# Kernel optimization log

Measured on AMD Instinct MI355X. Metric: run time of the kernel, lower is better.

The kernel has to match this reference:

```python
import jax, jax.numpy as jnp
import numpy as np

N_NODES = 170000
N_EDGES = 1200000
IN_DIM = 64
OUT_DIM = 40


def setup_inputs() -> dict:
    key = jax.random.key(0)
    k1, k2, k3, k4 = jax.random.split(key, 4)
    feats = jax.random.normal(k1, (N_NODES, IN_DIM), dtype=jnp.float32)
    # Linear layer params (Kaiming-ish scale)
    W = jax.random.normal(k2, (OUT_DIM, IN_DIM), dtype=jnp.float32) * (1.0 / np.sqrt(IN_DIM))
    b = jnp.zeros((OUT_DIM,), dtype=jnp.float32)
    src = jax.random.randint(k3, (N_EDGES,), 0, N_NODES, dtype=jnp.int64)
    dst = jax.random.randint(k4, (N_EDGES,), 0, N_NODES, dtype=jnp.int64)
    return {"feats": feats, "W": W, "b": b, "src": src, "dst": dst}


def reference(feats, W, b, src, dst):
    # DGL SGConv, k=1: symmetric normalization by in-degree^-1/2 on both sides.
    n = feats.shape[0]
    deg = jax.ops.segment_sum(jnp.ones_like(dst, dtype=feats.dtype), dst, num_segments=n)
    norm = jax.lax.rsqrt(jnp.maximum(deg, 1.0))  # clamp(min=1)
    h = feats * norm[:, None]                    # [N, D] pre-scale
    msgs = jnp.take(h, src, axis=0)              # [E, D] gather
    agg = jax.ops.segment_sum(msgs, dst, num_segments=n)  # [N, D] scatter-sum
    h = agg * norm[:, None]                      # post-scale
    out = jnp.einsum('nd,cd->nc', h, W) + b      # Linear(IN_DIM -> OUT_DIM)
    return out
```

## Files before the change

kernel.cpp:

```cpp
#include <hip/hip_runtime.h>
#include <hip/hip_bf16.h>

#define N_NODES 170000
#define N_EDGES 1200000
#define IN_DIM 64
#define OUT_DIM 40
#define PAD 32
#define ZW 20
#define MTILES (N_NODES / 16)
#define TFB ((MTILES + 3) / 4)
#define SEGS 8
#define SEG_SZ (N_NODES / SEGS)
#define SLICES 512
#define SLICE_E ((N_EDGES + SLICES - 1) / SLICES)
#define FILLB (SLICES * SEGS)
#define FUSED_BLOCKS (FILLB + TFB)
#define GWAVES (N_NODES / 2)
#define WS_DS32_OFF 36056576ULL
#define WS_SS32_OFF (WS_DS32_OFF + (size_t)N_EDGES * 4)
#define WS_NEED     (WS_SS32_OFF + (size_t)N_EDGES * 4)

typedef __attribute__((ext_vector_type(8))) short short8;
typedef __attribute__((ext_vector_type(4))) float f32x4;

__device__ __forceinline__ float bf2f(unsigned int u) {
    union { unsigned int i; float f; } v;
    v.i = u << 16;
    return v.f;
}

__device__ __forceinline__ unsigned short f2bf_bits(float x) {
    __hip_bfloat16 h = __float2bfloat16(x);
    union { __hip_bfloat16 h; unsigned short u; } c; c.h = h;
    return c.u;
}

__device__ __forceinline__ int load_idx(const void* p, int e, int is_i32) {
    return is_i32 ? ((const int*)p)[e] : (int)((const long long*)p)[e];
}

__global__ void __launch_bounds__(256) k_init(
    const unsigned short* __restrict__ Wraw, const unsigned short* __restrict__ braw,
    const unsigned int* __restrict__ dstraw, const unsigned int* __restrict__ srcraw,
    int* __restrict__ flags, unsigned short* __restrict__ Wb, float* __restrict__ bfv,
    int* __restrict__ cnt, int* __restrict__ ds32, int* __restrict__ ss32) {
    int tid = blockIdx.x * 256 + threadIdx.x;
    int gsz = (int)gridDim.x * 256;
    int4* c4 = (int4*)cnt;
    for (int i = tid; i < 42500; i += gsz) c4[i] = make_int4(0, 0, 0, 0);

    __shared__ int s_i32l;
    if (threadIdx.x == 0) s_i32l = 0;
    __syncthreads();
    if (dstraw[2 * threadIdx.x + 1] != 0u) atomicOr(&s_i32l, 1);
    __syncthreads();
    int is_i32 = s_i32l;

    if (!is_i32 && ds32) {
        const long long* d64 = (const long long*)dstraw;
        const long long* s64 = (const long long*)srcraw;
        for (int i = tid; i < N_EDGES; i += gsz) ds32[i] = (int)d64[i];
        for (int i = tid; i < N_EDGES; i += gsz) ss32[i] = (int)s64[i];
    }
    if (blockIdx.x != 0) return;

    __shared__ int s_f32;
    if (threadIdx.x == 0) s_f32 = 0;
    __syncthreads();
    for (int i = threadIdx.x; i < OUT_DIM * IN_DIM; i += 256) {
        float v = bf2f(Wraw[i]);
        if (!(fabsf(v) <= 100.0f)) atomicOr(&s_f32, 1);
    }
    __syncthreads();
    int is_f32 = s_f32;
    if (threadIdx.x == 0) { flags[0] = s_f32; flags[1] = is_i32; }
    for (int i = threadIdx.x; i < OUT_DIM * IN_DIM; i += 256)
        Wb[i] = is_f32 ? f2bf_bits(((const float*)Wraw)[i]) : Wraw[i];
    for (int i = threadIdx.x; i < OUT_DIM; i += 256)
        bfv[i] = is_f32 ? ((const float*)braw)[i] : bf2f(braw[i]);
}

__global__ void __launch_bounds__(256) k_fused(
    const void* __restrict__ src, const void* __restrict__ dst,
    int* __restrict__ cnt, int* __restrict__ slots,
    const void* __restrict__ feats, const unsigned short* __restrict__ Wb,
    unsigned short* __restrict__ Zp16, const int* __restrict__ flags,
    const int* __restrict__ ds32, const int* __restrict__ ss32) {
    int bid = blockIdx.x;
    int do_fill, id;
    if (bid < 2 * TFB) { do_fill = bid & 1; id = bid >> 1; }
    else               { do_fill = 1;       id = bid - TFB; }

    if (do_fill) {
        int is_i32 = flags[1];
        int seg   = id & 7;
        int slice = id >> 3;
        int lo = seg * SEG_SZ, hi = lo + SEG_SZ;
        int e0 = slice * SLICE_E;
        int e1 = e0 + SLICE_E; if (e1 > N_EDGES) e1 = N_EDGES;
        const int* dp = is_i32 ? (const int*)dst : ds32;
        const int* sp = is_i32 ? (const int*)src : ss32;
        if (dp) {
            int nE = e1 - e0;
            int nV = nE >> 2;
            const int4* dv = (const int4*)(dp + e0);
            const int4* sv = (const int4*)(sp + e0);
            for (int q = (int)threadIdx.x; q < nV; q += 256) {
                int4 d4 = dv[q];
                int4 s4 = sv[q];
                if (d4.x >= lo && d4.x < hi) {
                    int pos = atomicAdd(&cnt[d4.x], 1);
                    if (pos < PAD) slots[(size_t)d4.x * PAD + pos] = s4.x;
                }
                if (d4.y >= lo && d4.y < hi) {
                    int pos = atomicAdd(&cnt[d4.y], 1);
                    if (pos < PAD) slots[(size_t)d4.y * PAD + pos] = s4.y;
                }
                if (d4.z >= lo && d4.z < hi) {
                    int pos = atomicAdd(&cnt[d4.z], 1);
                    if (pos < PAD) slots[(size_t)d4.z * PAD + pos] = s4.z;
                }
                if (d4.w >= lo && d4.w < hi) {
                    int pos = atomicAdd(&cnt[d4.w], 1);
                    if (pos < PAD) slots[(size_t)d4.w * PAD + pos] = s4.w;
                }
            }
            int rem = nE & 3;
            if ((int)threadIdx.x < rem) {
                int e = e0 + (nV << 2) + (int)threadIdx.x;
                int d = dp[e];
                if (d >= lo && d < hi) {
                    int pos = atomicAdd(&cnt[d], 1);
                    if (pos < PAD) slots[(size_t)d * PAD + pos] = sp[e];
                }
            }
        } else {
            for (int e = e0 + (int)threadIdx.x; e < e1; e += 256) {
                int d = load_idx(dst, e, 0);
                if (d >= lo && d < hi) {
                    int s = load_idx(src, e, 0);
                    int pos = atomicAdd(&cnt[d], 1);
                    if (pos < PAD) slots[(size_t)d * PAD + pos] = s;
                }
            }
        }
    } else {
        int is_f32 = flags[0];
        int wave = id * 4 + (int)(threadIdx.x >> 6);
        int lane = threadIdx.x & 63;
        if (wave >= MTILES) return;
        int m = lane & 15;
        int quad = lane >> 4;
        int node0 = wave * 16;

        short8 a0, a1;
        if (is_f32) {
            const float* frow = (const float*)feats + (size_t)(node0 + m) * IN_DIM + quad * 8;
            float4 p0 = *(const float4*)(frow + 0);
            float4 p1 = *(const float4*)(frow + 4);
            float4 p2 = *(const float4*)(frow + 32);
            float4 p3 = *(const float4*)(frow + 36);
            a0[0] = (short)f2bf_bits(p0.x); a0[1] = (short)f2bf_bits(p0.y);
            a0[2] = (short)f2bf_bits(p0.z); a0[3] = (short)f2bf_bits(p0.w);
            a0[4] = (short)f2bf_bits(p1.x); a0[5] = (short)f2bf_bits(p1.y);
            a0[6] = (short)f2bf_bits(p1.z); a0[7] = (short)f2bf_bits(p1.w);
            a1[0] = (short)f2bf_bits(p2.x); a1[1] = (short)f2bf_bits(p2.y);
            a1[2] = (short)f2bf_bits(p2.z); a1[3] = (short)f2bf_bits(p2.w);
            a1[4] = (short)f2bf_bits(p3.x); a1[5] = (short)f2bf_bits(p3.y);
            a1[6] = (short)f2bf_bits(p3.z); a1[7] = (short)f2bf_bits(p3.w);
        } else {
            const unsigned short* frow = (const unsigned short*)feats + (size_t)(node0 + m) * IN_DIM + quad * 8;
            a0 = *(const short8*)(frow);
            a1 = *(const short8*)(frow + 32);
        }

        f32x4 c0 = {0.f, 0.f, 0.f, 0.f}, c1 = c0, c2 = c0;
#pragma unroll
        for (int t = 0; t < 3; t++) {
            int n = t * 16 + m;
            bool ok = (n < OUT_DIM);
            short8 b0, b1;
#pragma unroll
            for (int j = 0; j < 8; j++) { b0[j] = 0; b1[j] = 0; }
            if (ok) {
                const unsigned short* wrow = Wb + (size_t)n * IN_DIM + quad * 8;
                b0 = *(const short8*)(wrow);
                b1 = *(const short8*)(wrow + 32);
            }
            if (t == 0) {
                c0 = __builtin_amdgcn_mfma_f32_16x16x32_bf16(a0, b0, c0, 0, 0, 0);
                c0 = __builtin_amdgcn_mfma_f32_16x16x32_bf16(a1, b1, c0, 0, 0, 0);
            } else if (t == 1) {
                c1 = __builtin_amdgcn_mfma_f32_16x16x32_bf16(a0, b0, c1, 0, 0, 0);
                c1 = __builtin_amdgcn_mfma_f32_16x16x32_bf16(a1, b1, c1, 0, 0, 0);
            } else {
                c2 = __builtin_amdgcn_mfma_f32_16x16x32_bf16(a0, b0, c2, 0, 0, 0);
                c2 = __builtin_amdgcn_mfma_f32_16x16x32_bf16(a1, b1, c2, 0, 0, 0);
            }
        }

        int r0 = quad * 4;
#pragma unroll
        for (int r = 0; r < 4; r++) {
            size_t base = (size_t)(node0 + r0 + r) * OUT_DIM;
            Zp16[base + m]      = f2bf_bits(c0[r]);
            Zp16[base + 16 + m] = f2bf_bits(c1[r]);
            if (m < 8)
                Zp16[base + 32 + m] = f2bf_bits(c2[r]);
        }
    }
}

__global__ void __launch_bounds__(256) k_gather(
    const int* __restrict__ cnt, const int* __restrict__ slots,
    const unsigned int* __restrict__ Zp, const float* __restrict__ bfv,
    float* __restrict__ out) {
    int wid = (blockIdx.x * blockDim.x + threadIdx.x) >> 6;
    int lane = threadIdx.x & 63;
    if (wid >= GWAVES) return;
    int nA = wid * 2, nB = nA + 1;

    int deg_my = cnt[nA + (lane >> 5)];
    int deg_ot = __shfl(deg_my, lane ^ 32);
    int degA = (lane < 32) ? deg_my : deg_ot;
    int degB = (lane < 32) ? deg_ot : deg_my;
    int dcA = degA > PAD ? PAD : degA;
    int dcB = degB > PAD ? PAD : degB;
    int dcm = dcA > dcB ? dcA : dcB;

    int myslot = slots[(size_t)(nA + (lane >> 5)) * PAD + (lane & 31)];

    int grp = lane / 10;
    int g3 = grp - (grp >= 3 ? 3 : 0);
    int cidx = lane - grp * 10;
    bool lact = (grp < 6);
    int side = (grp >= 3);
    int dcS = side ? dcB : dcA;
    int sbase = side * 32;

    float a0 = 0.f, a1 = 0.f, a2 = 0.f, a3 = 0.f;
    if (dcm > 0) {
        int rounds = (dcm + 2) / 3;
        int e = g3;
        bool v = lact && (e < dcS);
        int s = __shfl(myslot, sbase + (v ? e : 0));
        s = v ? s : 0;
        uint2 r = *(const uint2*)(Zp + (size_t)s * ZW + 2 * cidx);
        int cdeg = cnt[s];
        for (int rd = 1; rd < rounds; rd++) {
            int e1 = rd * 3 + g3;
            bool v1 = lact && (e1 < dcS);
            int s1 = __shfl(myslot, sbase + (v1 ? e1 : 0));
            s1 = v1 ? s1 : 0;
            uint2 rn = *(const uint2*)(Zp + (size_t)s1 * ZW + 2 * cidx);
            int cn = cnt[s1];
            if (v) {
                float nvs = rsqrtf(cdeg > 1 ? (float)cdeg : 1.0f);
                a0 = fmaf(bf2f(r.x & 0xFFFFu), nvs, a0);
                a1 = fmaf(bf2f(r.x >> 16),     nvs, a1);
                a2 = fmaf(bf2f(r.y & 0xFFFFu), nvs, a2);
                a3 = fmaf(bf2f(r.y >> 16),     nvs, a3);
            }
            v = v1; r = rn; cdeg = cn;
        }
        if (v) {
            float nvs = rsqrtf(cdeg > 1 ? (float)cdeg : 1.0f);
            a0 = fmaf(bf2f(r.x & 0xFFFFu), nvs, a0);
            a1 = fmaf(bf2f(r.x >> 16),     nvs, a1);
            a2 = fmaf(bf2f(r.y & 0xFFFFu), nvs, a2);
            a3 = fmaf(bf2f(r.y >> 16),     nvs, a3);
        }
    }
    float t0 = a0 + __shfl(a0, (lane + 10) & 63) + __shfl(a0, (lane + 20) & 63);
    float t1 = a1 + __shfl(a1, (lane + 10) & 63) + __shfl(a1, (lane + 20) & 63);
    float t2 = a2 + __shfl(a2, (lane + 10) & 63) + __shfl(a2, (lane + 20) & 63);
    float t3 = a3 + __shfl(a3, (lane + 10) & 63) + __shfl(a3, (lane + 20) & 63);

    bool wA = (lane < 10);
    bool wB = (lane >= 30 && lane < 40);
    if (wA || wB) {
        int nOut = wA ? nA : nB;
        int ci   = wA ? lane : (lane - 30);
        int dg   = wA ? degA : degB;
        float nv = rsqrtf(dg > 1 ? (float)dg : 1.0f);
        float4 o;
        o.x = fmaf(t0, nv, bfv[4 * ci + 0]);
        o.y = fmaf(t1, nv, bfv[4 * ci + 1]);
        o.z = fmaf(t2, nv, bfv[4 * ci + 2]);
        o.w = fmaf(t3, nv, bfv[4 * ci + 3]);
        *reinterpret_cast<float4*>(out + (size_t)nOut * OUT_DIM + 4 * ci) = o;
    }
}

extern "C" void kernel_launch(void* const* d_in, const int* in_sizes, int n_in,
                              void* d_out, int out_size, void* d_ws, size_t ws_size,
                              hipStream_t stream) {
    const void* feats = d_in[0];
    const void* W     = d_in[1];
    const void* b     = d_in[2];
    const void* src   = d_in[3];
    const void* dst   = d_in[4];

    char* ws = (char*)d_ws;
    int*            flags = (int*)(ws + 0);
    float*          bfv   = (float*)(ws + 256);
    unsigned short* Wb    = (unsigned short*)(ws + 1024);
    int*            cnt   = (int*)(ws + 16384);
    int*            slots = (int*)(ws + 696448);
    unsigned short* Zp16  = (unsigned short*)(ws + 22456448);
    unsigned int*   Zp    = (unsigned int*)(ws + 22456448);
    int*            ds32  = (ws_size >= WS_NEED) ? (int*)(ws + WS_DS32_OFF) : nullptr;
    int*            ss32  = (ws_size >= WS_NEED) ? (int*)(ws + WS_SS32_OFF) : nullptr;

    k_init<<<1024, 256, 0, stream>>>((const unsigned short*)W, (const unsigned short*)b,
                                     (const unsigned int*)dst, (const unsigned int*)src,
                                     flags, Wb, bfv, cnt, ds32, ss32);
    k_fused<<<FUSED_BLOCKS, 256, 0, stream>>>(src, dst, cnt, slots, feats, Wb, Zp16, flags, ds32, ss32);
    k_gather<<<(GWAVES * 64 + 255) / 256, 256, 0, stream>>>(cnt, slots, Zp, bfv, (float*)d_out);
}
```

Baseline: 196.5 us.

## Merge init, fill/transform, and gather into one cooperative persistent kernel

```diff
diff --git a/kernel.cpp b/kernel.cpp
--- a/kernel.cpp
+++ b/kernel.cpp
@@ -1,5 +1,8 @@
 #include <hip/hip_runtime.h>
 #include <hip/hip_bf16.h>
+#include <hip/hip_cooperative_groups.h>
+
+namespace cg = cooperative_groups;
 
 #define N_NODES 170000
 #define N_EDGES 1200000
@@ -14,8 +17,9 @@
 #define SLICES 512
 #define SLICE_E ((N_EDGES + SLICES - 1) / SLICES)
 #define FILLB (SLICES * SEGS)
-#define FUSED_BLOCKS (FILLB + TFB)
+#define FUSED_UNITS (FILLB + TFB)
 #define GWAVES (N_NODES / 2)
+#define GCHUNKS (GWAVES / 4)
 #define WS_DS32_OFF 36056576ULL
 #define WS_SS32_OFF (WS_DS32_OFF + (size_t)N_EDGES * 4)
 #define WS_NEED     (WS_SS32_OFF + (size_t)N_EDGES * 4)
@@ -39,185 +43,134 @@
     return is_i32 ? ((const int*)p)[e] : (int)((const long long*)p)[e];
 }
 
-__global__ void __launch_bounds__(256) k_init(
-    const unsigned short* __restrict__ Wraw, const unsigned short* __restrict__ braw,
-    const unsigned int* __restrict__ dstraw, const unsigned int* __restrict__ srcraw,
-    int* __restrict__ flags, unsigned short* __restrict__ Wb, float* __restrict__ bfv,
-    int* __restrict__ cnt, int* __restrict__ ds32, int* __restrict__ ss32) {
-    int tid = blockIdx.x * 256 + threadIdx.x;
-    int gsz = (int)gridDim.x * 256;
-    int4* c4 = (int4*)cnt;
-    for (int i = tid; i < 42500; i += gsz) c4[i] = make_int4(0, 0, 0, 0);
-
-    __shared__ int s_i32l;
-    if (threadIdx.x == 0) s_i32l = 0;
-    __syncthreads();
-    if (dstraw[2 * threadIdx.x + 1] != 0u) atomicOr(&s_i32l, 1);
-    __syncthreads();
-    int is_i32 = s_i32l;
-
-    if (!is_i32 && ds32) {
-        const long long* d64 = (const long long*)dstraw;
-        const long long* s64 = (const long long*)srcraw;
-        for (int i = tid; i < N_EDGES; i += gsz) ds32[i] = (int)d64[i];
-        for (int i = tid; i < N_EDGES; i += gsz) ss32[i] = (int)s64[i];
-    }
-    if (blockIdx.x != 0) return;
-
-    __shared__ int s_f32;
-    if (threadIdx.x == 0) s_f32 = 0;
-    __syncthreads();
-    for (int i = threadIdx.x; i < OUT_DIM * IN_DIM; i += 256) {
-        float v = bf2f(Wraw[i]);
-        if (!(fabsf(v) <= 100.0f)) atomicOr(&s_f32, 1);
-    }
-    __syncthreads();
-    int is_f32 = s_f32;
-    if (threadIdx.x == 0) { flags[0] = s_f32; flags[1] = is_i32; }
-    for (int i = threadIdx.x; i < OUT_DIM * IN_DIM; i += 256)
-        Wb[i] = is_f32 ? f2bf_bits(((const float*)Wraw)[i]) : Wraw[i];
-    for (int i = threadIdx.x; i < OUT_DIM; i += 256)
-        bfv[i] = is_f32 ? ((const float*)braw)[i] : bf2f(braw[i]);
-}
-
-__global__ void __launch_bounds__(256) k_fused(
-    const void* __restrict__ src, const void* __restrict__ dst,
-    int* __restrict__ cnt, int* __restrict__ slots,
-    const void* __restrict__ feats, const unsigned short* __restrict__ Wb,
-    unsigned short* __restrict__ Zp16, const int* __restrict__ flags,
-    const int* __restrict__ ds32, const int* __restrict__ ss32) {
-    int bid = blockIdx.x;
-    int do_fill, id;
-    if (bid < 2 * TFB) { do_fill = bid & 1; id = bid >> 1; }
-    else               { do_fill = 1;       id = bid - TFB; }
-
-    if (do_fill) {
-        int is_i32 = flags[1];
-        int seg   = id & 7;
-        int slice = id >> 3;
-        int lo = seg * SEG_SZ, hi = lo + SEG_SZ;
-        int e0 = slice * SLICE_E;
-        int e1 = e0 + SLICE_E; if (e1 > N_EDGES) e1 = N_EDGES;
-        const int* dp = is_i32 ? (const int*)dst : ds32;
-        const int* sp = is_i32 ? (const int*)src : ss32;
-        if (dp) {
-            int nE = e1 - e0;
-            int nV = nE >> 2;
-            const int4* dv = (const int4*)(dp + e0);
-            const int4* sv = (const int4*)(sp + e0);
-            for (int q = (int)threadIdx.x; q < nV; q += 256) {
-                int4 d4 = dv[q];
-                int4 s4 = sv[q];
-                if (d4.x >= lo && d4.x < hi) {
-                    int pos = atomicAdd(&cnt[d4.x], 1);
-                    if (pos < PAD) slots[(size_t)d4.x * PAD + pos] = s4.x;
-                }
-                if (d4.y >= lo && d4.y < hi) {
-                    int pos = atomicAdd(&cnt[d4.y], 1);
-                    if (pos < PAD) slots[(size_t)d4.y * PAD + pos] = s4.y;
-                }
-                if (d4.z >= lo && d4.z < hi) {
-                    int pos = atomicAdd(&cnt[d4.z], 1);
-                    if (pos < PAD) slots[(size_t)d4.z * PAD + pos] = s4.z;
-                }
-                if (d4.w >= lo && d4.w < hi) {
-                    int pos = atomicAdd(&cnt[d4.w], 1);
-                    if (pos < PAD) slots[(size_t)d4.w * PAD + pos] = s4.w;
-                }
-            }
-            int rem = nE & 3;
-            if ((int)threadIdx.x < rem) {
-                int e = e0 + (nV << 2) + (int)threadIdx.x;
-                int d = dp[e];
-                if (d >= lo && d < hi) {
-                    int pos = atomicAdd(&cnt[d], 1);
-                    if (pos < PAD) slots[(size_t)d * PAD + pos] = sp[e];
-                }
-            }
+
+__device__ __forceinline__ void fill_unit(
+    int id, int is_i32, const void* src, const void* dst,
+    const int* dp_, const int* sp_, int* cnt, int* slots) {
+    int seg   = id & 7;
+    int slice = id >> 3;
+    int lo = seg * SEG_SZ, hi = lo + SEG_SZ;
+    int e0 = slice * SLICE_E;
+    int e1 = e0 + SLICE_E; if (e1 > N_EDGES) e1 = N_EDGES;
+    const int* dp = is_i32 ? (const int*)dst : dp_;
+    const int* sp = is_i32 ? (const int*)src : sp_;
+    if (dp) {
+        int nE = e1 - e0;
+        int nV = nE >> 2;
+        const int4* dv = (const int4*)(dp + e0);
+        const int4* sv = (const int4*)(sp + e0);
+        for (int q = (int)threadIdx.x; q < nV; q += 256) {
+            int4 d4 = dv[q];
+            int4 s4 = sv[q];
+            if (d4.x >= lo && d4.x < hi) {
+                int pos = atomicAdd(&cnt[d4.x], 1);
+                if (pos < PAD) slots[(size_t)d4.x * PAD + pos] = s4.x;
+            }
+            if (d4.y >= lo && d4.y < hi) {
+                int pos = atomicAdd(&cnt[d4.y], 1);
+                if (pos < PAD) slots[(size_t)d4.y * PAD + pos] = s4.y;
+            }
+            if (d4.z >= lo && d4.z < hi) {
+                int pos = atomicAdd(&cnt[d4.z], 1);
+                if (pos < PAD) slots[(size_t)d4.z * PAD + pos] = s4.z;
+            }
+            if (d4.w >= lo && d4.w < hi) {
+                int pos = atomicAdd(&cnt[d4.w], 1);
+                if (pos < PAD) slots[(size_t)d4.w * PAD + pos] = s4.w;
+            }
+        }
+        int rem = nE & 3;
+        if ((int)threadIdx.x < rem) {
+            int e = e0 + (nV << 2) + (int)threadIdx.x;
+            int d = dp[e];
+            if (d >= lo && d < hi) {
+                int pos = atomicAdd(&cnt[d], 1);
+                if (pos < PAD) slots[(size_t)d * PAD + pos] = sp[e];
+            }
+        }
+    } else {
+        for (int e = e0 + (int)threadIdx.x; e < e1; e += 256) {
+            int d = load_idx(dst, e, 0);
+            if (d >= lo && d < hi) {
+                int s = load_idx(src, e, 0);
+                int pos = atomicAdd(&cnt[d], 1);
+                if (pos < PAD) slots[(size_t)d * PAD + pos] = s;
+            }
+        }
+    }
+}
+
+__device__ __forceinline__ void transform_unit(
+    int id, int is_f32, const void* feats, const unsigned short* Wb,
+    unsigned short* Zp16) {
+    int wave = id * 4 + (int)(threadIdx.x >> 6);
+    int lane = threadIdx.x & 63;
+    if (wave >= MTILES) return;
+    int m = lane & 15;
+    int quad = lane >> 4;
+    int node0 = wave * 16;
+
+    short8 a0, a1;
+    if (is_f32) {
+        const float* frow = (const float*)feats + (size_t)(node0 + m) * IN_DIM + quad * 8;
+        float4 p0 = *(const float4*)(frow + 0);
+        float4 p1 = *(const float4*)(frow + 4);
+        float4 p2 = *(const float4*)(frow + 32);
+        float4 p3 = *(const float4*)(frow + 36);
+        a0[0] = (short)f2bf_bits(p0.x); a0[1] = (short)f2bf_bits(p0.y);
+        a0[2] = (short)f2bf_bits(p0.z); a0[3] = (short)f2bf_bits(p0.w);
+        a0[4] = (short)f2bf_bits(p1.x); a0[5] = (short)f2bf_bits(p1.y);
+        a0[6] = (short)f2bf_bits(p1.z); a0[7] = (short)f2bf_bits(p1.w);
+        a1[0] = (short)f2bf_bits(p2.x); a1[1] = (short)f2bf_bits(p2.y);
+        a1[2] = (short)f2bf_bits(p2.z); a1[3] = (short)f2bf_bits(p2.w);
+        a1[4] = (short)f2bf_bits(p3.x); a1[5] = (short)f2bf_bits(p3.y);
+        a1[6] = (short)f2bf_bits(p3.z); a1[7] = (short)f2bf_bits(p3.w);
+    } else {
+        const unsigned short* frow = (const unsigned short*)feats + (size_t)(node0 + m) * IN_DIM + quad * 8;
+        a0 = *(const short8*)(frow);
+        a1 = *(const short8*)(frow + 32);
+    }
+
+    f32x4 c0 = {0.f, 0.f, 0.f, 0.f}, c1 = c0, c2 = c0;
+#pragma unroll
+    for (int t = 0; t < 3; t++) {
+        int n = t * 16 + m;
+        bool ok = (n < OUT_DIM);
+        short8 b0, b1;
+#pragma unroll
+        for (int j = 0; j < 8; j++) { b0[j] = 0; b1[j] = 0; }
+        if (ok) {
+            const unsigned short* wrow = Wb + (size_t)n * IN_DIM + quad * 8;
+            b0 = *(const short8*)(wrow);
+            b1 = *(const short8*)(wrow + 32);
+        }
+        if (t == 0) {
+            c0 = __builtin_amdgcn_mfma_f32_16x16x32_bf16(a0, b0, c0, 0, 0, 0);
+            c0 = __builtin_amdgcn_mfma_f32_16x16x32_bf16(a1, b1, c0, 0, 0, 0);
+        } else if (t == 1) {
+            c1 = __builtin_amdgcn_mfma_f32_16x16x32_bf16(a0, b0, c1, 0, 0, 0);
+            c1 = __builtin_amdgcn_mfma_f32_16x16x32_bf16(a1, b1, c1, 0, 0, 0);
         } else {
-            for (int e = e0 + (int)threadIdx.x; e < e1; e += 256) {
-                int d = load_idx(dst, e, 0);
-                if (d >= lo && d < hi) {
-                    int s = load_idx(src, e, 0);
-                    int pos = atomicAdd(&cnt[d], 1);
-                    if (pos < PAD) slots[(size_t)d * PAD + pos] = s;
-                }
-            }
-        }
-    } else {
-        int is_f32 = flags[0];
-        int wave = id * 4 + (int)(threadIdx.x >> 6);
-        int lane = threadIdx.x & 63;
-        if (wave >= MTILES) return;
-        int m = lane & 15;
-        int quad = lane >> 4;
-        int node0 = wave * 16;
-
-        short8 a0, a1;
-        if (is_f32) {
-            const float* frow = (const float*)feats + (size_t)(node0 + m) * IN_DIM + quad * 8;
-            float4 p0 = *(const float4*)(frow + 0);
-            float4 p1 = *(const float4*)(frow + 4);
-            float4 p2 = *(const float4*)(frow + 32);
-            float4 p3 = *(const float4*)(frow + 36);
-            a0[0] = (short)f2bf_bits(p0.x); a0[1] = (short)f2bf_bits(p0.y);
-            a0[2] = (short)f2bf_bits(p0.z); a0[3] = (short)f2bf_bits(p0.w);
-            a0[4] = (short)f2bf_bits(p1.x); a0[5] = (short)f2bf_bits(p1.y);
-            a0[6] = (short)f2bf_bits(p1.z); a0[7] = (short)f2bf_bits(p1.w);
-            a1[0] = (short)f2bf_bits(p2.x); a1[1] = (short)f2bf_bits(p2.y);
-            a1[2] = (short)f2bf_bits(p2.z); a1[3] = (short)f2bf_bits(p2.w);
-            a1[4] = (short)f2bf_bits(p3.x); a1[5] = (short)f2bf_bits(p3.y);
-            a1[6] = (short)f2bf_bits(p3.z); a1[7] = (short)f2bf_bits(p3.w);
-        } else {
-            const unsigned short* frow = (const unsigned short*)feats + (size_t)(node0 + m) * IN_DIM + quad * 8;
-            a0 = *(const short8*)(frow);
-            a1 = *(const short8*)(frow + 32);
-        }
-
-        f32x4 c0 = {0.f, 0.f, 0.f, 0.f}, c1 = c0, c2 = c0;
+            c2 = __builtin_amdgcn_mfma_f32_16x16x32_bf16(a0, b0, c2, 0, 0, 0);
+            c2 = __builtin_amdgcn_mfma_f32_16x16x32_bf16(a1, b1, c2, 0, 0, 0);
+        }
+    }
+
+    int r0 = quad * 4;
 #pragma unroll
-        for (int t = 0; t < 3; t++) {
-            int n = t * 16 + m;
-            bool ok = (n < OUT_DIM);
-            short8 b0, b1;
-#pragma unroll
-            for (int j = 0; j < 8; j++) { b0[j] = 0; b1[j] = 0; }
-            if (ok) {
-                const unsigned short* wrow = Wb + (size_t)n * IN_DIM + quad * 8;
-                b0 = *(const short8*)(wrow);
-                b1 = *(const short8*)(wrow + 32);
-            }
-            if (t == 0) {
-                c0 = __builtin_amdgcn_mfma_f32_16x16x32_bf16(a0, b0, c0, 0, 0, 0);
-                c0 = __builtin_amdgcn_mfma_f32_16x16x32_bf16(a1, b1, c0, 0, 0, 0);
-            } else if (t == 1) {
-                c1 = __builtin_amdgcn_mfma_f32_16x16x32_bf16(a0, b0, c1, 0, 0, 0);
-                c1 = __builtin_amdgcn_mfma_f32_16x16x32_bf16(a1, b1, c1, 0, 0, 0);
-            } else {
-                c2 = __builtin_amdgcn_mfma_f32_16x16x32_bf16(a0, b0, c2, 0, 0, 0);
-                c2 = __builtin_amdgcn_mfma_f32_16x16x32_bf16(a1, b1, c2, 0, 0, 0);
-            }
-        }
-
-        int r0 = quad * 4;
-#pragma unroll
-        for (int r = 0; r < 4; r++) {
-            size_t base = (size_t)(node0 + r0 + r) * OUT_DIM;
-            Zp16[base + m]      = f2bf_bits(c0[r]);
-            Zp16[base + 16 + m] = f2bf_bits(c1[r]);
-            if (m < 8)
-                Zp16[base + 32 + m] = f2bf_bits(c2[r]);
-        }
-    }
-}
-
-__global__ void __launch_bounds__(256) k_gather(
-    const int* __restrict__ cnt, const int* __restrict__ slots,
-    const unsigned int* __restrict__ Zp, const float* __restrict__ bfv,
-    float* __restrict__ out) {
-    int wid = (blockIdx.x * blockDim.x + threadIdx.x) >> 6;
+    for (int r = 0; r < 4; r++) {
+        size_t base = (size_t)(node0 + r0 + r) * OUT_DIM;
+        Zp16[base + m]      = f2bf_bits(c0[r]);
+        Zp16[base + 16 + m] = f2bf_bits(c1[r]);
+        if (m < 8)
+            Zp16[base + 32 + m] = f2bf_bits(c2[r]);
+    }
+}
+
+__device__ __forceinline__ void gather_wid(
+    int wid, const int* cnt, const int* slots, const unsigned int* Zp,
+    const float* bfv, float* out) {
     int lane = threadIdx.x & 63;
-    if (wid >= GWAVES) return;
     int nA = wid * 2, nB = nA + 1;
 
     int deg_my = cnt[nA + (lane >> 5)];
@@ -292,6 +245,135 @@
     }
 }
 
+__global__ void __launch_bounds__(256) k_mega(
+    const void* __restrict__ feats, const unsigned short* __restrict__ Wraw,
+    const unsigned short* __restrict__ braw, const void* __restrict__ src,
+    const void* __restrict__ dst, char* __restrict__ ws,
+    float* __restrict__ out, int has_cvt) {
+    float*          bfv   = (float*)(ws + 256);
+    unsigned short* Wb    = (unsigned short*)(ws + 1024);
+    int*            cnt   = (int*)(ws + 16384);
+    int*            slots = (int*)(ws + 696448);
+    unsigned short* Zp16  = (unsigned short*)(ws + 22456448);
+    const unsigned int* Zp = (const unsigned int*)Zp16;
+    int* ds32 = has_cvt ? (int*)(ws + WS_DS32_OFF) : nullptr;
+    int* ss32 = has_cvt ? (int*)(ws + WS_SS32_OFF) : nullptr;
+
+    int G   = (int)gridDim.x;
+    int tid = (int)blockIdx.x * 256 + (int)threadIdx.x;
+    int gsz = G * 256;
+
+    __shared__ int sh_i32, sh_f32;
+    if (threadIdx.x == 0) { sh_i32 = 0; sh_f32 = 0; }
+    __syncthreads();
+    {
+        const unsigned int* dstraw = (const unsigned int*)dst;
+        if (dstraw[2 * threadIdx.x + 1] != 0u) atomicOr(&sh_i32, 1);
+    }
+    for (int i = threadIdx.x; i < OUT_DIM * IN_DIM; i += 256) {
+        float v = bf2f(Wraw[i]);
+        if (!(fabsf(v) <= 100.0f)) atomicOr(&sh_f32, 1);
+    }
+    int4* c4 = (int4*)cnt;
+    for (int i = tid; i < 42500; i += gsz) c4[i] = make_int4(0, 0, 0, 0);
+    __syncthreads();
+    int is_i32 = sh_i32, is_f32 = sh_f32;
+
+    if (!is_i32 && ds32) {
+        const long long* d64 = (const long long*)dst;
+        const long long* s64 = (const long long*)src;
+        for (int i = tid; i < N_EDGES; i += gsz) ds32[i] = (int)d64[i];
+        for (int i = tid; i < N_EDGES; i += gsz) ss32[i] = (int)s64[i];
+    }
+    if (blockIdx.x == 0) {
+        for (int i = threadIdx.x; i < OUT_DIM * IN_DIM; i += 256)
+            Wb[i] = is_f32 ? f2bf_bits(((const float*)Wraw)[i]) : Wraw[i];
+        for (int i = threadIdx.x; i < OUT_DIM; i += 256)
+            bfv[i] = is_f32 ? ((const float*)braw)[i] : bf2f(braw[i]);
+    }
+
+    cg::this_grid().sync();
+
+    for (int u = (int)blockIdx.x; u < FUSED_UNITS; u += G) {
+        int do_fill, id;
+        if (u < 2 * TFB) { do_fill = u & 1; id = u >> 1; }
+        else             { do_fill = 1;     id = u - TFB; }
+        if (do_fill) fill_unit(id, is_i32, src, dst, ds32, ss32, cnt, slots);
+        else         transform_unit(id, is_f32, feats, Wb, Zp16);
+    }
+
+    cg::this_grid().sync();
+
+    for (int c = (int)blockIdx.x; c < GCHUNKS; c += G) {
+        int wid = c * 4 + (int)(threadIdx.x >> 6);
+        gather_wid(wid, cnt, slots, Zp, bfv, out);
+    }
+}
+
+__global__ void __launch_bounds__(256) k_init(
+    const unsigned short* __restrict__ Wraw, const unsigned short* __restrict__ braw,
+    const unsigned int* __restrict__ dstraw, const unsigned int* __restrict__ srcraw,
+    int* __restrict__ flags, unsigned short* __restrict__ Wb, float* __restrict__ bfv,
+    int* __restrict__ cnt, int* __restrict__ ds32, int* __restrict__ ss32) {
+    int tid = blockIdx.x * 256 + threadIdx.x;
+    int gsz = (int)gridDim.x * 256;
+    int4* c4 = (int4*)cnt;
+    for (int i = tid; i < 42500; i += gsz) c4[i] = make_int4(0, 0, 0, 0);
+
+    __shared__ int s_i32l;
+    if (threadIdx.x == 0) s_i32l = 0;
+    __syncthreads();
+    if (dstraw[2 * threadIdx.x + 1] != 0u) atomicOr(&s_i32l, 1);
+    __syncthreads();
+    int is_i32 = s_i32l;
+
+    if (!is_i32 && ds32) {
+        const long long* d64 = (const long long*)dstraw;
+        const long long* s64 = (const long long*)srcraw;
+        for (int i = tid; i < N_EDGES; i += gsz) ds32[i] = (int)d64[i];
+        for (int i = tid; i < N_EDGES; i += gsz) ss32[i] = (int)s64[i];
+    }
+    if (blockIdx.x != 0) return;
+
+    __shared__ int s_f32;
+    if (threadIdx.x == 0) s_f32 = 0;
+    __syncthreads();
+    for (int i = threadIdx.x; i < OUT_DIM * IN_DIM; i += 256) {
+        float v = bf2f(Wraw[i]);
+        if (!(fabsf(v) <= 100.0f)) atomicOr(&s_f32, 1);
+    }
+    __syncthreads();
+    int is_f32 = s_f32;
+    if (threadIdx.x == 0) { flags[0] = s_f32; flags[1] = is_i32; }
+    for (int i = threadIdx.x; i < OUT_DIM * IN_DIM; i += 256)
+        Wb[i] = is_f32 ? f2bf_bits(((const float*)Wraw)[i]) : Wraw[i];
+    for (int i = threadIdx.x; i < OUT_DIM; i += 256)
+        bfv[i] = is_f32 ? ((const float*)braw)[i] : bf2f(braw[i]);
+}
+
+__global__ void __launch_bounds__(256) k_fused(
+    const void* __restrict__ src, const void* __restrict__ dst,
+    int* __restrict__ cnt, int* __restrict__ slots,
+    const void* __restrict__ feats, const unsigned short* __restrict__ Wb,
+    unsigned short* __restrict__ Zp16, const int* __restrict__ flags,
+    const int* __restrict__ ds32, const int* __restrict__ ss32) {
+    int bid = blockIdx.x;
+    int do_fill, id;
+    if (bid < 2 * TFB) { do_fill = bid & 1; id = bid >> 1; }
+    else               { do_fill = 1;       id = bid - TFB; }
+    if (do_fill) fill_unit(id, flags[1], src, dst, ds32, ss32, cnt, slots);
+    else         transform_unit(id, flags[0], feats, Wb, Zp16);
+}
+
+__global__ void __launch_bounds__(256) k_gather(
+    const int* __restrict__ cnt, const int* __restrict__ slots,
+    const unsigned int* __restrict__ Zp, const float* __restrict__ bfv,
+    float* __restrict__ out) {
+    int wid = (blockIdx.x * blockDim.x + threadIdx.x) >> 6;
+    if (wid >= GWAVES) return;
+    gather_wid(wid, cnt, slots, Zp, bfv, out);
+}
+
 extern "C" void kernel_launch(void* const* d_in, const int* in_sizes, int n_in,
                               void* d_out, int out_size, void* d_ws, size_t ws_size,
                               hipStream_t stream) {
@@ -302,6 +384,35 @@
     const void* dst   = d_in[4];
 
     char* ws = (char*)d_ws;
+    float* outp = (float*)d_out;
+    int has_cvt = (ws_size >= WS_NEED) ? 1 : 0;
+
+    static int coop_state = -1;
+    static int coop_grid  = 0;
+    if (coop_state != 0) {
+        if (coop_grid == 0) {
+            int nb = 0;
+            if (hipOccupancyMaxActiveBlocksPerMultiprocessor(&nb, (const void*)k_mega, 256, 0)
+                    != hipSuccess || nb < 1) nb = 4;
+            if (nb > 8) nb = 8;
+            coop_grid = nb * 256;
+            if (coop_grid > 2048) coop_grid = 2048;
+        }
+        const void*           a0 = feats;
+        const unsigned short* a1 = (const unsigned short*)W;
+        const unsigned short* a2 = (const unsigned short*)b;
+        const void*           a3 = src;
+        const void*           a4 = dst;
+        char*                 a5 = ws;
+        float*                a6 = outp;
+        int                   a7 = has_cvt;
+        void* kargs[] = {&a0, &a1, &a2, &a3, &a4, &a5, &a6, &a7};
+        hipError_t err = hipLaunchCooperativeKernel((const void*)k_mega, dim3(coop_grid),
+                                                    dim3(256), kargs, 0, stream);
+        if (err == hipSuccess) { coop_state = 1; return; }
+        coop_state = 0;
+    }
+
     int*            flags = (int*)(ws + 0);
     float*          bfv   = (float*)(ws + 256);
     unsigned short* Wb    = (unsigned short*)(ws + 1024);
@@ -309,12 +420,12 @@
     int*            slots = (int*)(ws + 696448);
     unsigned short* Zp16  = (unsigned short*)(ws + 22456448);
     unsigned int*   Zp    = (unsigned int*)(ws + 22456448);
-    int*            ds32  = (ws_size >= WS_NEED) ? (int*)(ws + WS_DS32_OFF) : nullptr;
-    int*            ss32  = (ws_size >= WS_NEED) ? (int*)(ws + WS_SS32_OFF) : nullptr;
+    int*            ds32  = has_cvt ? (int*)(ws + WS_DS32_OFF) : nullptr;
+    int*            ss32  = has_cvt ? (int*)(ws + WS_SS32_OFF) : nullptr;
 
     k_init<<<1024, 256, 0, stream>>>((const unsigned short*)W, (const unsigned short*)b,
                                      (const unsigned int*)dst, (const unsigned int*)src,
                                      flags, Wb, bfv, cnt, ds32, ss32);
-    k_fused<<<FUSED_BLOCKS, 256, 0, stream>>>(src, dst, cnt, slots, feats, Wb, Zp16, flags, ds32, ss32);
-    k_gather<<<(GWAVES * 64 + 255) / 256, 256, 0, stream>>>(cnt, slots, Zp, bfv, (float*)d_out);
-}
+    k_fused<<<FUSED_UNITS, 256, 0, stream>>>(src, dst, cnt, slots, feats, Wb, Zp16, flags, ds32, ss32);
+    k_gather<<<(GWAVES * 64 + 255) / 256, 256, 0, stream>>>(cnt, slots, Zp, bfv, outp);
+}
```

Result: slower. 459.9 us (+134.0%).
